# Performance work log

Measured on AMD Instinct MI355X. Metric: run time of the kernel, lower is better.

Reference implementation:

```python
import jax, jax.numpy as jnp
import numpy as np

B, H, W, C = 32, 56, 56, 384
NH, WS, SS = 12, 7, 3
HD = C // NH
HID = 4 * C
N = WS * WS
NW = (H // WS) * (W // WS)


def _rel_pos_index():
    coords = np.stack(np.meshgrid(np.arange(WS), np.arange(WS), indexing='ij')).reshape(2, -1)
    rel = (coords[:, :, None] - coords[:, None, :]).transpose(1, 2, 0)
    rel[..., 0] += WS - 1
    rel[..., 1] += WS - 1
    rel[..., 0] *= 2 * WS - 1
    return rel.sum(-1)  # (N, N) int


def _shift_mask():
    img = np.zeros((H, W))
    cnt = 0
    sl = (slice(0, -WS), slice(-WS, -SS), slice(-SS, None))
    for hs in sl:
        for ws_ in sl:
            img[hs, ws_] = cnt
            cnt += 1
    mw = img.reshape(H // WS, WS, W // WS, WS).transpose(0, 2, 1, 3).reshape(-1, N)
    diff = mw[:, None, :] - mw[:, :, None]  # (nW, N, N)
    return np.where(diff != 0, -100.0, 0.0).astype(np.float32)


_REL_IDX = _rel_pos_index()
_MASK = _shift_mask()


def _ln(x, g, b, eps=1e-5):
    m = jnp.mean(x, -1, keepdims=True)
    v = jnp.mean(jnp.square(x - m), -1, keepdims=True)
    return (x - m) * jax.lax.rsqrt(v + eps) * g + b


def setup_inputs() -> dict:
    key = jax.random.key(0)
    ks = jax.random.split(key, 8)
    s = 0.02
    return {
        'x': jax.random.normal(ks[0], (B, H * W, C), jnp.float32),
        'ln1_g': jnp.ones((C,)), 'ln1_b': jnp.zeros((C,)),
        'qkv_w': jax.random.normal(ks[1], (C, 3 * C)) * s, 'qkv_b': jnp.zeros((3 * C,)),
        'rel_bias': jax.random.normal(ks[2], ((2 * WS - 1) ** 2, NH)) * s,
        'proj_w': jax.random.normal(ks[3], (C, C)) * s, 'proj_b': jnp.zeros((C,)),
        'ln2_g': jnp.ones((C,)), 'ln2_b': jnp.zeros((C,)),
        'fc1_w': jax.random.normal(ks[4], (C, HID)) * s, 'fc1_b': jnp.zeros((HID,)),
        'fc2_w': jax.random.normal(ks[5], (HID, C)) * s, 'fc2_b': jnp.zeros((C,)),
    }


def _forward(x, ln1_g, ln1_b, qkv_w, qkv_b, rel_bias, proj_w, proj_b,
             ln2_g, ln2_b, fc1_w, fc1_b, fc2_w, fc2_b):
    mask = jnp.asarray(_MASK)
    shortcut = x
    y = _ln(x, ln1_g, ln1_b).reshape(B, H, W, C)
    y = jnp.roll(y, (-SS, -SS), axis=(1, 2))
    # window partition -> (B*nW, N, C)
    y = y.reshape(B, H // WS, WS, W // WS, WS, C).transpose(0, 1, 3, 2, 4, 5)
    win = y.reshape(-1, N, C)
    Bn = win.shape[0]
    qkv = (win @ qkv_w + qkv_b).reshape(Bn, N, 3, NH, HD).transpose(2, 0, 3, 1, 4)
    q, k, v = qkv[0] * (HD ** -0.5), qkv[1], qkv[2]  # (Bn, NH, N, HD)
    attn = jnp.einsum('whid,whjd->whij', q, k)
    bias = rel_bias[_REL_IDX.reshape(-1)].reshape(N, N, NH).transpose(2, 0, 1)
    attn = attn + bias[None]
    attn = attn.reshape(B, NW, NH, N, N) + mask[None, :, None]
    attn = jax.nn.softmax(attn.reshape(Bn, NH, N, N), axis=-1)
    out = jnp.einsum('whij,whjd->whid', attn, v).transpose(0, 2, 1, 3).reshape(Bn, N, C)
    out = out @ proj_w + proj_b
    # window reverse + roll back
    out = out.reshape(B, H // WS, W // WS, WS, WS, C).transpose(0, 1, 3, 2, 4, 5).reshape(B, H, W, C)
    out = jnp.roll(out, (SS, SS), axis=(1, 2)).reshape(B, H * W, C)
    x = shortcut + out
    h = jax.nn.gelu(_ln(x, ln2_g, ln2_b) @ fc1_w + fc1_b, approximate=False)
    ffn = jax.nn.gelu(h @ fc2_w + fc2_b, approximate=False)  # repo MLP has act after 2nd linear
    return x + ffn


def reference(x, ln1_g, ln1_b, qkv_w, qkv_b, rel_bias, proj_w, proj_b,
              ln2_g, ln2_b, fc1_w, fc1_b, fc2_w, fc2_b):
    return _forward(x, ln1_g, ln1_b, qkv_w, qkv_b, rel_bias, proj_w, proj_b,
                    ln2_g, ln2_b, fc1_w, fc1_b, fc2_w, fc2_b)
```

## Files before the change

### kernel.cpp

```cpp
#include <hip/hip_runtime.h>
#include <hip/hip_bf16.h>
#include <cstdint>
#include <cstddef>


typedef __attribute__((ext_vector_type(8))) short bf16x8;
typedef __attribute__((ext_vector_type(4))) float f32x4;

__device__ __forceinline__ float bf2f(__hip_bfloat16 x) { return __bfloat162float(x); }
__device__ __forceinline__ __hip_bfloat16 f2bf(float x) { return __float2bfloat16(x); }
__device__ __forceinline__ float s2f(short s) {
    unsigned u = ((unsigned)(unsigned short)s) << 16;
    return __builtin_bit_cast(float, u);
}
__device__ __forceinline__ short f2s(float f) {
    __hip_bfloat16 h = __float2bfloat16(f);
    return (short)__builtin_bit_cast(unsigned short, h);
}
__device__ __forceinline__ float gelu_exact(float x) {
    return 0.5f * x * (1.0f + erff(x * 0.70710678118654752f));
}

__global__ __launch_bounds__(256)
void ln_stats_bf16(const __hip_bfloat16* __restrict__ src, float* __restrict__ stats)
{
    int t = blockIdx.x * 4 + (threadIdx.x >> 6);
    int lane = threadIdx.x & 63;
    const __hip_bfloat16* p = src + (size_t)t * 384 + lane * 6;
    float s = 0.f, s2 = 0.f;
#pragma unroll
    for (int u = 0; u < 6; ++u) { float f = bf2f(p[u]); s += f; s2 += f * f; }
#pragma unroll
    for (int off = 32; off > 0; off >>= 1) { s += __shfl_xor(s, off); s2 += __shfl_xor(s2, off); }
    if (lane == 0) {
        float mean = s * (1.f / 384.f);
        float var  = fmaxf(s2 * (1.f / 384.f) - mean * mean, 0.f);
        stats[2 * t]     = mean;
        stats[2 * t + 1] = rsqrtf(var + 1e-5f);
    }
}

__global__ __launch_bounds__(256)
void wconv_kernel(const float* __restrict__ W, __hip_bfloat16* __restrict__ Wt,
                  int K, int N, int total)
{
    int idx = blockIdx.x * 256 + threadIdx.x;
    if (idx >= total) return;
    int k = idx / N, n = idx - k * N;
    Wt[(size_t)n * K + k] = f2bf(W[idx]);
}

__global__ __launch_bounds__(256)
void ln1_gather_kernel(const float* __restrict__ x,
                       const float* __restrict__ g,
                       const float* __restrict__ bb,
                       __hip_bfloat16* __restrict__ wbuf)
{
    int wrow = blockIdx.x * 4 + (threadIdx.x >> 6);
    int lane = threadIdx.x & 63;
    int bi = wrow / 49, n = wrow - bi * 49;
    int b_ = bi >> 6, wid = bi & 63;
    int wh = wid >> 3, ww = wid & 7;
    int r = n / 7, c = n - (n / 7) * 7;
    int sh = wh * 7 + r + 3; if (sh >= 56) sh -= 56;
    int sw = ww * 7 + c + 3; if (sw >= 56) sw -= 56;
    const float* p = x + (size_t)(b_ * 3136 + sh * 56 + sw) * 384 + lane * 6;
    float v[6];
    float2 v01 = *(const float2*)p;
    float2 v23 = *(const float2*)(p + 2);
    float2 v45 = *(const float2*)(p + 4);
    v[0] = v01.x; v[1] = v01.y; v[2] = v23.x; v[3] = v23.y; v[4] = v45.x; v[5] = v45.y;
    float s = 0.f, s2 = 0.f;
#pragma unroll
    for (int u = 0; u < 6; ++u) { s += v[u]; s2 += v[u] * v[u]; }
#pragma unroll
    for (int off = 32; off > 0; off >>= 1) { s += __shfl_xor(s, off); s2 += __shfl_xor(s2, off); }
    float mean = s * (1.f / 384.f);
    float var  = fmaxf(s2 * (1.f / 384.f) - mean * mean, 0.f);
    float rstd = rsqrtf(var + 1e-5f);
    __hip_bfloat16* dst = wbuf + (size_t)wrow * 384 + lane * 6;
#pragma unroll
    for (int u = 0; u < 6; ++u) {
        int ch = lane * 6 + u;
        dst[u] = f2bf((v[u] - mean) * rstd * g[ch] + bb[ch]);
    }
}

__global__ __launch_bounds__(256)
void attn_kernel(const __hip_bfloat16* __restrict__ qkv,
                 const float* __restrict__ rel_bias,
                 __hip_bfloat16* __restrict__ attn_out,
                 int win_base)
{
    const int wi = blockIdx.x / 12;
    const int nh = blockIdx.x - wi * 12;
    const int gwin = win_base + wi;
    const int wid = gwin & 63;
    const int wh = wid >> 3, ww = wid & 7;
    const int tid = threadIdx.x;

    __shared__ alignas(16) float sQ[49 * 36];
    __shared__ alignas(16) float sK[49 * 36];
    __shared__ alignas(16) float sV[49 * 36];
    __shared__ float sS[49 * 49];
    __shared__ float sBias[169];
    __shared__ unsigned char sGrp[49];

    for (int idx = tid; idx < 169; idx += 256) sBias[idx] = rel_bias[idx * 12 + nh];
    if (tid < 49) {
        int r = tid / 7, c = tid - (tid / 7) * 7;
        int gh = (wh == 7) ? ((r < 4) ? 1 : 2) : 0;
        int gw = (ww == 7) ? ((c < 4) ? 1 : 2) : 0;
        sGrp[tid] = (unsigned char)(gh * 3 + gw);
    }
    for (int s = tid; s < 588; s += 256) {
        int which = s / 196, rem = s - which * 196;
        int row = rem >> 2, seg = rem & 3;
        bf16x8 vv = *(const bf16x8*)(qkv + (size_t)(wi * 49 + row) * 1152
                                     + which * 384 + nh * 32 + seg * 8);
        float* dstp = (which == 0 ? sQ : which == 1 ? sK : sV) + row * 36 + seg * 8;
#pragma unroll
        for (int e = 0; e < 8; ++e) dstp[e] = s2f(vv[e]);
    }
    __syncthreads();

    for (int idx = tid; idx < 2401; idx += 256) {
        int i = idx / 49, j = idx - (idx / 49) * 49;
        const float* qp = sQ + i * 36;
        const float* kp = sK + j * 36;
        float acc = 0.f;
#pragma unroll
        for (int d = 0; d < 32; ++d) acc += qp[d] * kp[d];
        int ri = i / 7, ci = i - (i / 7) * 7;
        int rj = j / 7, cj = j - (j / 7) * 7;
        float bias = sBias[(ri - rj + 6) * 13 + (ci - cj + 6)];
        float msk = (sGrp[i] == sGrp[j]) ? 0.f : -100.f;
        sS[idx] = acc * 0.17677669529663689f + bias + msk;
    }
    __syncthreads();

    if (tid < 196) {
        int i = tid >> 2, l4 = tid & 3;
        float mx = -1e30f;
        for (int j = l4; j < 49; j += 4) mx = fmaxf(mx, sS[i * 49 + j]);
        mx = fmaxf(mx, __shfl_xor(mx, 1, 4));
        mx = fmaxf(mx, __shfl_xor(mx, 2, 4));
        float sum = 0.f;
        for (int j = l4; j < 49; j += 4) {
            float e = expf(sS[i * 49 + j] - mx);
            sS[i * 49 + j] = e; sum += e;
        }
        sum += __shfl_xor(sum, 1, 4);
        sum += __shfl_xor(sum, 2, 4);
        float inv = 1.f / sum;
        for (int j = l4; j < 49; j += 4) sS[i * 49 + j] *= inv;
    }
    __syncthreads();

    __hip_bfloat16* dst = attn_out + (size_t)gwin * 49 * 384 + nh * 32;
    for (int idx = tid; idx < 1568; idx += 256) {
        int i = idx >> 5, d = idx & 31;
        const float* sp = sS + i * 49;
        float acc = 0.f;
#pragma unroll
        for (int j = 0; j < 49; ++j) acc += sp[j] * sV[j * 36 + d];
        dst[(size_t)i * 384 + d] = f2bf(acc);
    }
}

template<int MODE>
__global__ __launch_bounds__(256)
void gemm_mfma(const __hip_bfloat16* __restrict__ A,
               const __hip_bfloat16* __restrict__ Bt,
               const float* __restrict__ bias,
               const float* __restrict__ x_in,
               const float* __restrict__ lnst,
               const float* __restrict__ ln_g,
               const float* __restrict__ ln_b,
               const __hip_bfloat16* __restrict__ res,
               __hip_bfloat16* __restrict__ out_h,
               float* __restrict__ out_f,
               int N, int K, int m_base)
{
    __shared__ alignas(16) char smem[128 * 136 * 2];
    __hip_bfloat16* As = (__hip_bfloat16*)smem;
    __hip_bfloat16* Bs = (__hip_bfloat16*)(smem + 10240);
    __hip_bfloat16* Cs = (__hip_bfloat16*)smem;

    const int tid = threadIdx.x;

    const int nwg = gridDim.x * gridDim.y;
    int orig = blockIdx.y * gridDim.x + blockIdx.x;
    int q = nwg >> 3, r = nwg & 7;
    int xcd = orig & 7, pos = orig >> 3;
    int id = xcd * q + ((xcd < r) ? xcd : r) + pos;
    const int bm = id / gridDim.x;
    const int bn = id - bm * gridDim.x;

    const int lane = tid & 63;
    const int w = tid >> 6, wr = w >> 1, wc = w & 1;
    const int fr = lane & 15, fq = lane >> 4;

    f32x4 acc[4][4] = {};

    const int r0 = tid >> 2, ks0 = tid & 3;
    const int r1 = r0 + 64;
    const __hip_bfloat16* Aptr0 = A + (size_t)(bm * 128 + r0) * K + ks0 * 8;
    const __hip_bfloat16* Aptr1 = A + (size_t)(bm * 128 + r1) * K + ks0 * 8;
    const __hip_bfloat16* Bptr0 = Bt + (size_t)(bn * 128 + r0) * K + ks0 * 8;
    const __hip_bfloat16* Bptr1 = Bt + (size_t)(bn * 128 + r1) * K + ks0 * 8;

    float lm0 = 0.f, lr0 = 0.f, lm1 = 0.f, lr1 = 0.f;
    if (MODE == 1) {
        lm0 = lnst[2 * (bm * 128 + r0)]; lr0 = lnst[2 * (bm * 128 + r0) + 1];
        lm1 = lnst[2 * (bm * 128 + r1)]; lr1 = lnst[2 * (bm * 128 + r1) + 1];
    }

    for (int kk = 0; kk < K; kk += 32) {
        bf16x8 a0 = *(const bf16x8*)(Aptr0 + kk);
        bf16x8 a1 = *(const bf16x8*)(Aptr1 + kk);
        bf16x8 b0 = *(const bf16x8*)(Bptr0 + kk);
        bf16x8 b1 = *(const bf16x8*)(Bptr1 + kk);
        if (MODE == 1) {
            float4 g0 = *(const float4*)(ln_g + kk + ks0 * 8);
            float4 g1 = *(const float4*)(ln_g + kk + ks0 * 8 + 4);
            float4 c0 = *(const float4*)(ln_b + kk + ks0 * 8);
            float4 c1 = *(const float4*)(ln_b + kk + ks0 * 8 + 4);
            float gv[8] = {g0.x, g0.y, g0.z, g0.w, g1.x, g1.y, g1.z, g1.w};
            float cv[8] = {c0.x, c0.y, c0.z, c0.w, c1.x, c1.y, c1.z, c1.w};
#pragma unroll
            for (int e = 0; e < 8; ++e) {
                a0[e] = f2s((s2f(a0[e]) - lm0) * lr0 * gv[e] + cv[e]);
                a1[e] = f2s((s2f(a1[e]) - lm1) * lr1 * gv[e] + cv[e]);
            }
        }
        __syncthreads();
        *(bf16x8*)&As[r0 * 40 + ks0 * 8] = a0;
        *(bf16x8*)&As[r1 * 40 + ks0 * 8] = a1;
        *(bf16x8*)&Bs[r0 * 40 + ks0 * 8] = b0;
        *(bf16x8*)&Bs[r1 * 40 + ks0 * 8] = b1;
        __syncthreads();
        bf16x8 af[4], bfv[4];
#pragma unroll
        for (int mi = 0; mi < 4; ++mi)
            af[mi] = *(const bf16x8*)&As[(wr * 64 + mi * 16 + fr) * 40 + fq * 8];
#pragma unroll
        for (int ni = 0; ni < 4; ++ni)
            bfv[ni] = *(const bf16x8*)&Bs[(wc * 64 + ni * 16 + fr) * 40 + fq * 8];
#pragma unroll
        for (int mi = 0; mi < 4; ++mi)
#pragma unroll
            for (int ni = 0; ni < 4; ++ni)
                acc[mi][ni] = __builtin_amdgcn_mfma_f32_16x16x32_bf16(
                    af[mi], bfv[ni], acc[mi][ni], 0, 0, 0);
    }

    const int mrow0 = bm * 128 + wr * 64;
    const int ncol0 = bn * 128 + wc * 64;
    float bias_v[4];
#pragma unroll
    for (int ni = 0; ni < 4; ++ni) bias_v[ni] = bias[ncol0 + ni * 16 + fr];

    if (MODE == 1 || MODE == 3) {
        __syncthreads();
#pragma unroll
        for (int mi = 0; mi < 4; ++mi)
#pragma unroll
            for (int rr = 0; rr < 4; ++rr) {
                int row = wr * 64 + mi * 16 + fq * 4 + rr;
#pragma unroll
                for (int ni = 0; ni < 4; ++ni) {
                    int col = wc * 64 + ni * 16 + fr;
                    float v = acc[mi][ni][rr] + bias_v[ni];
                    Cs[row * 136 + col] = f2bf(MODE == 1 ? gelu_exact(v) : v);
                }
            }
        __syncthreads();
        int row = tid >> 1, half = tid & 1;
        size_t o = (size_t)(bm * 128 + row) * N + bn * 128 + half * 64;
        const __hip_bfloat16* src = &Cs[row * 136 + half * 64];
#pragma unroll
        for (int j = 0; j < 8; ++j)
            *(bf16x8*)(out_h + o + j * 8) = *(const bf16x8*)(src + j * 8);
        return;
    }

#pragma unroll
    for (int mi = 0; mi < 4; ++mi) {
#pragma unroll
        for (int rr = 0; rr < 4; ++rr) {
            int m = mrow0 + mi * 16 + fq * 4 + rr;
            if (MODE == 0) {
                int biw = m / 49, n_ = m - biw * 49;
                int b_ = biw >> 6, wid = biw & 63;
                int wh = wid >> 3, ww = wid & 7;
                int rw = n_ / 7, cc = n_ - (n_ / 7) * 7;
                int h = wh * 7 + rw + 3; if (h >= 56) h -= 56;
                int wcol = ww * 7 + cc + 3; if (wcol >= 56) wcol -= 56;
                size_t drow = (size_t)(b_ * 3136 + h * 56 + wcol) * 384;
#pragma unroll
                for (int ni = 0; ni < 4; ++ni) {
                    int nc = ncol0 + ni * 16 + fr;
                    float v = acc[mi][ni][rr] + bias_v[ni];
                    out_h[drow + nc] = f2bf(x_in[drow + nc] + v);
                }
            } else {
                size_t og = (size_t)(m_base + m) * 384;
                size_t ol = (size_t)m * 384;
#pragma unroll
                for (int ni = 0; ni < 4; ++ni) {
                    int nc = ncol0 + ni * 16 + fr;
                    out_f[og + nc] = bf2f(res[ol + nc])
                                   + gelu_exact(acc[mi][ni][rr] + bias_v[ni]);
                }
            }
        }
    }
}

extern "C" void kernel_launch(void* const* d_in, const int* in_sizes, int n_in,
                              void* d_out, int out_size, void* d_ws, size_t ws_size,
                              hipStream_t stream)
{
    (void)in_sizes; (void)n_in; (void)out_size; (void)ws_size;
    const float* x      = (const float*)d_in[0];
    const float* ln1_g  = (const float*)d_in[1];
    const float* ln1_b  = (const float*)d_in[2];
    const float* qkv_w  = (const float*)d_in[3];
    const float* qkv_b  = (const float*)d_in[4];
    const float* rel_b  = (const float*)d_in[5];
    const float* proj_w = (const float*)d_in[6];
    const float* proj_b = (const float*)d_in[7];
    const float* ln2_g  = (const float*)d_in[8];
    const float* ln2_b  = (const float*)d_in[9];
    const float* fc1_w  = (const float*)d_in[10];
    const float* fc1_b  = (const float*)d_in[11];
    const float* fc2_w  = (const float*)d_in[12];
    const float* fc2_b  = (const float*)d_in[13];
    float* out = (float*)d_out;

    __hip_bfloat16* aout = (__hip_bfloat16*)d_out;
    __hip_bfloat16* wbuf = (__hip_bfloat16*)((char*)d_out + 77070336);
    __hip_bfloat16* xmid = wbuf;

    char* ws = (char*)d_ws;
    float* ln2s = (float*)ws;
    __hip_bfloat16* qkv_wt  = (__hip_bfloat16*)(ws + 802816);
    __hip_bfloat16* proj_wt = (__hip_bfloat16*)(ws + 1687552);
    __hip_bfloat16* fc1_wt  = (__hip_bfloat16*)(ws + 1982464);
    __hip_bfloat16* fc2_wt  = (__hip_bfloat16*)(ws + 3162112);
    __hip_bfloat16* qkvbuf  = (__hip_bfloat16*)(ws + 4341760);
    __hip_bfloat16* hbuf    = (__hip_bfloat16*)(ws + 4341760);
    __hip_bfloat16* resb    = (__hip_bfloat16*)(ws + 4341760 + 38535168);

    wconv_kernel<<<1728, 256, 0, stream>>>(qkv_w,  qkv_wt,  384, 1152, 442368);
    wconv_kernel<<<576,  256, 0, stream>>>(proj_w, proj_wt, 384, 384,  147456);
    wconv_kernel<<<2304, 256, 0, stream>>>(fc1_w,  fc1_wt,  384, 1536, 589824);
    wconv_kernel<<<2304, 256, 0, stream>>>(fc2_w,  fc2_wt,  1536, 384, 589824);

    ln1_gather_kernel<<<25088, 256, 0, stream>>>(x, ln1_g, ln1_b, wbuf);

    for (int c = 0; c < 8; ++c) {
        size_t mb = (size_t)c * 12544;
        gemm_mfma<3><<<dim3(9, 98), 256, 0, stream>>>(
            wbuf + mb * 384, qkv_wt, qkv_b, nullptr, nullptr, nullptr, nullptr, nullptr,
            qkvbuf, nullptr, 1152, 384, 0);
        attn_kernel<<<3072, 256, 0, stream>>>(qkvbuf, rel_b, aout, c * 256);
    }

    gemm_mfma<0><<<dim3(3, 784), 256, 0, stream>>>(
        aout, proj_wt, proj_b, x, nullptr, nullptr, nullptr, nullptr,
        xmid, nullptr, 384, 384, 0);

    ln_stats_bf16<<<25088, 256, 0, stream>>>(xmid, ln2s);

    for (int c = 0; c < 8; ++c) {
        size_t mb = (size_t)c * 12544;
        gemm_mfma<1><<<dim3(12, 98), 256, 0, stream>>>(
            xmid + mb * 384, fc1_wt, fc1_b, nullptr, ln2s + 2 * mb, ln2_g, ln2_b, nullptr,
            hbuf, nullptr, 1536, 384, 0);
        if (c < 7) {
            gemm_mfma<2><<<dim3(3, 98), 256, 0, stream>>>(
                hbuf, fc2_wt, fc2_b, nullptr, nullptr, nullptr, nullptr,
                xmid + mb * 384, nullptr, out, 384, 1536, (int)mb);
        } else {
            hipMemcpyAsync(resb, xmid + (size_t)94080 * 384, (size_t)6272 * 384 * 2,
                           hipMemcpyDeviceToDevice, stream);
            gemm_mfma<2><<<dim3(3, 49), 256, 0, stream>>>(
                hbuf, fc2_wt, fc2_b, nullptr, nullptr, nullptr, nullptr,
                xmid + (size_t)87808 * 384, nullptr, out, 384, 1536, 87808);
            gemm_mfma<2><<<dim3(3, 49), 256, 0, stream>>>(
                hbuf + (size_t)6272 * 1536, fc2_wt, fc2_b, nullptr, nullptr, nullptr, nullptr,
                resb, nullptr, out, 384, 1536, 94080);
        }
    }
}
```

Before: 1.869 ms.

## Pipeline GEMM with triple-buffered direct global-to-LDS loads and tiled weight transpose

The GEMM main loop now loads A and B tiles straight from global memory into LDS with global_load_lds, three stages deep, so copies overlap with MFMA work instead of going through registers between two barriers per step. The LayerNorm fold in MODE 1 moves to the fragment registers after the LDS read, with gamma, beta and the row statistics cached in shared memory. Output stores become nontemporal, and weight conversion uses an LDS-tiled transpose for coalesced access. The unpadded LDS layout may cause bank conflicts, and the hand-written vmcnt waits depend on an exact count of outstanding loads.

```diff
diff --git a/kernel.cpp b/kernel.cpp
--- a/kernel.cpp
+++ b/kernel.cpp
@@ -19,6 +19,11 @@
 }
 __device__ __forceinline__ float gelu_exact(float x) {
     return 0.5f * x * (1.0f + erff(x * 0.70710678118654752f));
+}
+__device__ __forceinline__ void gl_lds(const void* g, void* l) {
+    __builtin_amdgcn_global_load_lds(
+        (const __attribute__((address_space(1))) unsigned int*)g,
+        (__attribute__((address_space(3))) unsigned int*)l, 16, 0, 0);
 }
 
 __global__ __launch_bounds__(256)
@@ -41,13 +46,24 @@
 }
 
 __global__ __launch_bounds__(256)
-void wconv_kernel(const float* __restrict__ W, __hip_bfloat16* __restrict__ Wt,
-                  int K, int N, int total)
-{
-    int idx = blockIdx.x * 256 + threadIdx.x;
-    if (idx >= total) return;
-    int k = idx / N, n = idx - k * N;
-    Wt[(size_t)n * K + k] = f2bf(W[idx]);
+void wconv_t(const float* __restrict__ W, __hip_bfloat16* __restrict__ Wt, int K, int N)
+{
+    __shared__ float tile[64][65];
+    const int n0 = blockIdx.x * 64, k0 = blockIdx.y * 64;
+    const int tid = threadIdx.x;
+#pragma unroll
+    for (int i = 0; i < 16; ++i) {
+        int kk = (tid >> 6) + i * 4;
+        int nn = tid & 63;
+        tile[kk][nn] = W[(size_t)(k0 + kk) * N + n0 + nn];
+    }
+    __syncthreads();
+#pragma unroll
+    for (int i = 0; i < 16; ++i) {
+        int nn = (tid >> 6) + i * 4;
+        int kk = tid & 63;
+        Wt[(size_t)(n0 + nn) * K + k0 + kk] = f2bf(tile[kk][nn]);
+    }
 }
 
 __global__ __launch_bounds__(256)
@@ -182,10 +198,12 @@
                float* __restrict__ out_f,
                int N, int K, int m_base)
 {
-    __shared__ alignas(16) char smem[128 * 136 * 2];
-    __hip_bfloat16* As = (__hip_bfloat16*)smem;
-    __hip_bfloat16* Bs = (__hip_bfloat16*)(smem + 10240);
+    __shared__ alignas(16) char smem[49152 + 4096];
     __hip_bfloat16* Cs = (__hip_bfloat16*)smem;
+    float* sMean = (float*)(smem + 49152);
+    float* sRstd = (float*)(smem + 49152 + 512);
+    float* sG    = (float*)(smem + 49152 + 1024);
+    float* sB2   = (float*)(smem + 49152 + 2560);
 
     const int tid = threadIdx.x;
 
@@ -203,66 +221,98 @@
 
     f32x4 acc[4][4] = {};
 
-    const int r0 = tid >> 2, ks0 = tid & 3;
-    const int r1 = r0 + 64;
-    const __hip_bfloat16* Aptr0 = A + (size_t)(bm * 128 + r0) * K + ks0 * 8;
-    const __hip_bfloat16* Aptr1 = A + (size_t)(bm * 128 + r1) * K + ks0 * 8;
-    const __hip_bfloat16* Bptr0 = Bt + (size_t)(bn * 128 + r0) * K + ks0 * 8;
-    const __hip_bfloat16* Bptr1 = Bt + (size_t)(bn * 128 + r1) * K + ks0 * 8;
-
-    float lm0 = 0.f, lr0 = 0.f, lm1 = 0.f, lr1 = 0.f;
+    const int srow = w * 16 + (lane >> 2);
+    const int sseg = lane & 3;
+    const __hip_bfloat16* Ag = A + (size_t)(bm * 128 + srow) * K + sseg * 8;
+    const __hip_bfloat16* Bg = Bt + (size_t)(bn * 128 + srow) * K + sseg * 8;
+    const size_t rowskip = (size_t)64 * K;
+
+    float lnm[4], lnr[4];
     if (MODE == 1) {
-        lm0 = lnst[2 * (bm * 128 + r0)]; lr0 = lnst[2 * (bm * 128 + r0) + 1];
-        lm1 = lnst[2 * (bm * 128 + r1)]; lr1 = lnst[2 * (bm * 128 + r1) + 1];
-    }
-
-    for (int kk = 0; kk < K; kk += 32) {
-        bf16x8 a0 = *(const bf16x8*)(Aptr0 + kk);
-        bf16x8 a1 = *(const bf16x8*)(Aptr1 + kk);
-        bf16x8 b0 = *(const bf16x8*)(Bptr0 + kk);
-        bf16x8 b1 = *(const bf16x8*)(Bptr1 + kk);
+        for (int i = tid; i < 128; i += 256) {
+            sMean[i] = lnst[2 * (bm * 128 + i)];
+            sRstd[i] = lnst[2 * (bm * 128 + i) + 1];
+        }
+        for (int i = tid; i < 384; i += 256) { sG[i] = ln_g[i]; sB2[i] = ln_b[i]; }
+        __syncthreads();
+#pragma unroll
+        for (int mi = 0; mi < 4; ++mi) {
+            int row = wr * 64 + mi * 16 + fr;
+            lnm[mi] = sMean[row]; lnr[mi] = sRstd[row];
+        }
+    }
+
+    const int mrow0 = bm * 128 + wr * 64;
+    const int ncol0 = bn * 128 + wc * 64;
+    float bias_v[4];
+#pragma unroll
+    for (int ni = 0; ni < 4; ++ni) bias_v[ni] = bias[ncol0 + ni * 16 + fr];
+
+    const int nt = K >> 5;
+#define STAGE(t_) do {                                                      \
+        const int kk_ = (t_) * 32;                                          \
+        char* b_ = smem + ((t_) % 3) * 16384 + w * 1024;                    \
+        gl_lds(Ag + kk_,           b_);                                     \
+        gl_lds(Ag + kk_ + rowskip, b_ + 4096);                              \
+        gl_lds(Bg + kk_,           b_ + 8192);                              \
+        gl_lds(Bg + kk_ + rowskip, b_ + 8192 + 4096);                       \
+    } while (0)
+
+    STAGE(0);
+    STAGE(1);
+
+    const int aoff = wr * 4096 + fr * 64 + fq * 16;
+    const int boff = wc * 4096 + fr * 64 + fq * 16;
+
+    for (int t = 0; t < nt; ++t) {
+        if (t + 2 < nt) {
+            STAGE(t + 2);
+            asm volatile("s_waitcnt vmcnt(8)" ::: "memory");
+        } else if (t + 1 < nt) {
+            asm volatile("s_waitcnt vmcnt(4)" ::: "memory");
+        } else {
+            asm volatile("s_waitcnt vmcnt(0)" ::: "memory");
+        }
+        __builtin_amdgcn_s_barrier();
+
+        const char* bA = smem + (t % 3) * 16384;
+        const char* bB = bA + 8192;
+        bf16x8 af[4], bfv[4];
+#pragma unroll
+        for (int mi = 0; mi < 4; ++mi)
+            af[mi] = *(const bf16x8*)(bA + aoff + mi * 1024);
+#pragma unroll
+        for (int ni = 0; ni < 4; ++ni)
+            bfv[ni] = *(const bf16x8*)(bB + boff + ni * 1024);
+
         if (MODE == 1) {
-            float4 g0 = *(const float4*)(ln_g + kk + ks0 * 8);
-            float4 g1 = *(const float4*)(ln_g + kk + ks0 * 8 + 4);
-            float4 c0 = *(const float4*)(ln_b + kk + ks0 * 8);
-            float4 c1 = *(const float4*)(ln_b + kk + ks0 * 8 + 4);
+            const int kkb = t * 32 + fq * 8;
+            float4 g0 = *(const float4*)(sG + kkb);
+            float4 g1 = *(const float4*)(sG + kkb + 4);
+            float4 c0 = *(const float4*)(sB2 + kkb);
+            float4 c1 = *(const float4*)(sB2 + kkb + 4);
             float gv[8] = {g0.x, g0.y, g0.z, g0.w, g1.x, g1.y, g1.z, g1.w};
             float cv[8] = {c0.x, c0.y, c0.z, c0.w, c1.x, c1.y, c1.z, c1.w};
 #pragma unroll
-            for (int e = 0; e < 8; ++e) {
-                a0[e] = f2s((s2f(a0[e]) - lm0) * lr0 * gv[e] + cv[e]);
-                a1[e] = f2s((s2f(a1[e]) - lm1) * lr1 * gv[e] + cv[e]);
-            }
-        }
-        __syncthreads();
-        *(bf16x8*)&As[r0 * 40 + ks0 * 8] = a0;
-        *(bf16x8*)&As[r1 * 40 + ks0 * 8] = a1;
-        *(bf16x8*)&Bs[r0 * 40 + ks0 * 8] = b0;
-        *(bf16x8*)&Bs[r1 * 40 + ks0 * 8] = b1;
-        __syncthreads();
-        bf16x8 af[4], bfv[4];
-#pragma unroll
-        for (int mi = 0; mi < 4; ++mi)
-            af[mi] = *(const bf16x8*)&As[(wr * 64 + mi * 16 + fr) * 40 + fq * 8];
-#pragma unroll
-        for (int ni = 0; ni < 4; ++ni)
-            bfv[ni] = *(const bf16x8*)&Bs[(wc * 64 + ni * 16 + fr) * 40 + fq * 8];
+            for (int mi = 0; mi < 4; ++mi)
+#pragma unroll
+                for (int e = 0; e < 8; ++e)
+                    af[mi][e] = f2s((s2f(af[mi][e]) - lnm[mi]) * lnr[mi] * gv[e] + cv[e]);
+        }
+
 #pragma unroll
         for (int mi = 0; mi < 4; ++mi)
 #pragma unroll
             for (int ni = 0; ni < 4; ++ni)
                 acc[mi][ni] = __builtin_amdgcn_mfma_f32_16x16x32_bf16(
                     af[mi], bfv[ni], acc[mi][ni], 0, 0, 0);
-    }
-
-    const int mrow0 = bm * 128 + wr * 64;
-    const int ncol0 = bn * 128 + wc * 64;
-    float bias_v[4];
-#pragma unroll
-    for (int ni = 0; ni < 4; ++ni) bias_v[ni] = bias[ncol0 + ni * 16 + fr];
+
+        asm volatile("s_waitcnt lgkmcnt(0)" ::: "memory");
+        __builtin_amdgcn_s_barrier();
+    }
+#undef STAGE
 
     if (MODE == 1 || MODE == 3) {
-        __syncthreads();
 #pragma unroll
         for (int mi = 0; mi < 4; ++mi)
 #pragma unroll
@@ -280,8 +330,11 @@
         size_t o = (size_t)(bm * 128 + row) * N + bn * 128 + half * 64;
         const __hip_bfloat16* src = &Cs[row * 136 + half * 64];
 #pragma unroll
-        for (int j = 0; j < 8; ++j)
-            *(bf16x8*)(out_h + o + j * 8) = *(const bf16x8*)(src + j * 8);
+        for (int j = 0; j < 8; ++j) {
+            bf16x8 v = *(const bf16x8*)(src + j * 8);
+            if (MODE == 1) __builtin_nontemporal_store(v, (bf16x8*)(out_h + o + j * 8));
+            else           *(bf16x8*)(out_h + o + j * 8) = v;
+        }
         return;
     }
 
@@ -302,7 +355,8 @@
                 for (int ni = 0; ni < 4; ++ni) {
                     int nc = ncol0 + ni * 16 + fr;
                     float v = acc[mi][ni][rr] + bias_v[ni];
-                    out_h[drow + nc] = f2bf(x_in[drow + nc] + v);
+                    __builtin_nontemporal_store(f2s(x_in[drow + nc] + v),
+                                                (short*)(out_h + drow + nc));
                 }
             } else {
                 size_t og = (size_t)(m_base + m) * 384;
@@ -310,8 +364,8 @@
 #pragma unroll
                 for (int ni = 0; ni < 4; ++ni) {
                     int nc = ncol0 + ni * 16 + fr;
-                    out_f[og + nc] = bf2f(res[ol + nc])
-                                   + gelu_exact(acc[mi][ni][rr] + bias_v[ni]);
+                    float v = bf2f(res[ol + nc]) + gelu_exact(acc[mi][ni][rr] + bias_v[ni]);
+                    __builtin_nontemporal_store(v, out_f + og + nc);
                 }
             }
         }
@@ -353,10 +407,10 @@
     __hip_bfloat16* hbuf    = (__hip_bfloat16*)(ws + 4341760);
     __hip_bfloat16* resb    = (__hip_bfloat16*)(ws + 4341760 + 38535168);
 
-    wconv_kernel<<<1728, 256, 0, stream>>>(qkv_w,  qkv_wt,  384, 1152, 442368);
-    wconv_kernel<<<576,  256, 0, stream>>>(proj_w, proj_wt, 384, 384,  147456);
-    wconv_kernel<<<2304, 256, 0, stream>>>(fc1_w,  fc1_wt,  384, 1536, 589824);
-    wconv_kernel<<<2304, 256, 0, stream>>>(fc2_w,  fc2_wt,  1536, 384, 589824);
+    wconv_t<<<dim3(18, 6), 256, 0, stream>>>(qkv_w,  qkv_wt,  384, 1152);
+    wconv_t<<<dim3(6,  6), 256, 0, stream>>>(proj_w, proj_wt, 384, 384);
+    wconv_t<<<dim3(24, 6), 256, 0, stream>>>(fc1_w,  fc1_wt,  384, 1536);
+    wconv_t<<<dim3(6, 24), 256, 0, stream>>>(fc2_w,  fc2_wt,  1536, 384);
 
     ln1_gather_kernel<<<25088, 256, 0, stream>>>(x, ln1_g, ln1_b, wbuf);
 
```

New measurement: 2.232 ms. 1.19x slower.
